# Optimization experiments

Hardware: AMD Instinct MI355X
Metric: run time of the kernel (lower is better)

The kernel has to match this reference:

```python
import jax, jax.numpy as jnp
from jax import lax
import numpy as np

H = 30          # LSTM_HID_SIZE
NOUT = 5        # ENC_NUM_OUT


def lstm_layer(x, W, b):
    """TF contrib LSTMCell over time. x: [B, T, D], W: [D+H, 4H] (i, j, f, o), forget_bias=1.0."""
    B = x.shape[0]
    c0 = jnp.zeros((B, H), x.dtype)
    h0 = jnp.zeros((B, H), x.dtype)

    def step(carry, xt):
        c, h = carry
        z = jnp.concatenate([xt, h], axis=-1) @ W + b
        i, j, f, o = jnp.split(z, 4, axis=-1)
        c = c * jax.nn.sigmoid(f + 1.0) + jax.nn.sigmoid(i) * jnp.tanh(j)
        h = jnp.tanh(c) * jax.nn.sigmoid(o)
        return (c, h), h

    _, hs = lax.scan(step, (c0, h0), jnp.swapaxes(x, 0, 1))  # hs: [T, B, H]
    return jnp.swapaxes(hs, 0, 1)


def setup_inputs() -> dict:
    key = jax.random.key(0)
    ks = jax.random.split(key, 13)
    B, T, D = 64, 2048, 256
    s = 0.1
    w = lambda k, shp: (jax.random.normal(k, shp, dtype=jnp.float32) * s)
    return {
        "seq": jax.random.normal(ks[0], (B, T, D), dtype=jnp.float32),
        # encoder stacked LSTM
        "enc_W1": w(ks[1], (D + H, 4 * H)), "enc_b1": jnp.zeros((4 * H,), jnp.float32),
        "enc_W2": w(ks[2], (H + H, 4 * H)), "enc_b2": jnp.zeros((4 * H,), jnp.float32),
        # encoder dense -> latent
        "enc_Wd": w(ks[3], (H, NOUT)), "enc_bd": jnp.zeros((NOUT,), jnp.float32),
        # decoder dense (dead code in original, kept for faithfulness)
        "dec_Wd": w(ks[4], (NOUT, NOUT)), "dec_bd": jnp.zeros((NOUT,), jnp.float32),
        # decoder stacked LSTM over zero inputs of width 1
        "dec_W1": w(ks[5], (1 + H, 4 * H)), "dec_b1": jnp.zeros((4 * H,), jnp.float32),
        "dec_W2": w(ks[6], (H + H, 4 * H)), "dec_b2": jnp.zeros((4 * H,), jnp.float32),
    }


def reference(seq, enc_W1, enc_b1, enc_W2, enc_b2, enc_Wd, enc_bd,
              dec_Wd, dec_bd, dec_W1, dec_b1, dec_W2, dec_b2):
    B, T, _ = seq.shape
    # ---- encoder: 2-layer LSTM, last timestep, tanh dense -> latent [B, 5]
    h1 = lstm_layer(seq, enc_W1, enc_b1)
    h2 = lstm_layer(h1, enc_W2, enc_b2)
    latent = jnp.tanh(h2[:, -1, :] @ enc_Wd + enc_bd)
    # ---- decoder dense on latent (unused downstream in the original graph)
    vec2 = jnp.tanh(latent @ dec_Wd + dec_bd)  # noqa: F841 (dead code, faithful to source)
    # ---- decoder: 2-layer LSTM over zeros [B, T, 1], zero initial state
    dec_in = jnp.zeros((B, T, 1), seq.dtype)
    d1 = lstm_layer(dec_in, dec_W1, dec_b1)
    d2 = lstm_layer(d1, dec_W2, dec_b2)
    dec_out = d2[:, :, -1]  # output[:, :, -1] -> [B, T]
    return dec_out, latent
```

## Files before the change

### kernel.cpp

```cpp
#include <hip/hip_runtime.h>


#define BB 64
#define TT 2048
#define DD 256
#define HH 30
#define GG 120
#define PRE_ELEMS (64u * 2048u * 120u)

__device__ __forceinline__ float fast_exp(float x) {
  return __builtin_amdgcn_exp2f(x * 1.442695040888963f);
}
__device__ __forceinline__ float fast_rcp(float x) {
  return __builtin_amdgcn_rcpf(x);
}
__device__ __forceinline__ float sigm(float x) {
  return fast_rcp(1.0f + fast_exp(-x));
}
__device__ __forceinline__ float tanh_f(float x) {
  return 1.0f - 2.0f * fast_rcp(1.0f + fast_exp(2.0f * x));
}

__global__ __launch_bounds__(256) void gemm_pre(const float* __restrict__ A,
                                                const float* __restrict__ W,
                                                const float* __restrict__ bias,
                                                float* __restrict__ out) {
  __shared__ __align__(16) float sA[32 * 132];
  __shared__ __align__(16) float sW[32 * 120];
  const int tid = threadIdx.x;
  const int row0 = blockIdx.x * 128;
  const int tx = tid % 30;
  const int ty = tid / 30;
  const bool comp = tid < 240;
  float4 acc[16];
#pragma unroll
  for (int i = 0; i < 16; ++i) acc[i] = make_float4(0.f, 0.f, 0.f, 0.f);
  const float4* A4 = (const float4*)A;
  const float4* W4 = (const float4*)W;
  const int rload = tid >> 3;
  const int kq = tid & 7;
  for (int k0 = 0; k0 < 256; k0 += 32) {
    __syncthreads();
#pragma unroll
    for (int it = 0; it < 4; ++it) {
      int idx = tid + it * 256;
      if (idx < 960) ((float4*)sW)[idx] = W4[k0 * 30 + idx];
    }
#pragma unroll
    for (int m = 0; m < 4; ++m) {
      int rr = rload + m * 32;
      float4 v = A4[(size_t)(row0 + rr) * 64 + (k0 >> 2) + kq];
      int kk = kq * 4;
      sA[(kk + 0) * 132 + rr] = v.x;
      sA[(kk + 1) * 132 + rr] = v.y;
      sA[(kk + 2) * 132 + rr] = v.z;
      sA[(kk + 3) * 132 + rr] = v.w;
    }
    __syncthreads();
    if (comp) {
#pragma unroll 4
      for (int k = 0; k < 32; ++k) {
        const float4 w = ((const float4*)sW)[k * 30 + tx];
        const float4* a4 = (const float4*)&sA[k * 132 + ty * 16];
        float4 a0 = a4[0], a1 = a4[1], a2 = a4[2], a3 = a4[3];
        float av[16] = {a0.x, a0.y, a0.z, a0.w, a1.x, a1.y, a1.z, a1.w,
                        a2.x, a2.y, a2.z, a2.w, a3.x, a3.y, a3.z, a3.w};
#pragma unroll
        for (int i = 0; i < 16; ++i) {
          acc[i].x = fmaf(av[i], w.x, acc[i].x);
          acc[i].y = fmaf(av[i], w.y, acc[i].y);
          acc[i].z = fmaf(av[i], w.z, acc[i].z);
          acc[i].w = fmaf(av[i], w.w, acc[i].w);
        }
      }
    }
  }
  if (comp) {
    const float4 bv = ((const float4*)bias)[tx];
#pragma unroll
    for (int i = 0; i < 16; ++i) {
      int row = row0 + ty * 16 + i;
      float4 r;
      r.x = acc[i].x + bv.x;
      r.y = acc[i].y + bv.y;
      r.z = acc[i].z + bv.z;
      r.w = acc[i].w + bv.w;
      ((float4*)out)[(size_t)row * 30 + tx] = r;
    }
  }
}

__global__ __launch_bounds__(128, 1) void scan_kernel(
    const float* __restrict__ pre, const float* __restrict__ enc_W1,
    const float* __restrict__ enc_W2, const float* __restrict__ enc_b2,
    const float* __restrict__ enc_Wd, const float* __restrict__ enc_bd,
    const float* __restrict__ dec_W1, const float* __restrict__ dec_b1,
    const float* __restrict__ dec_W2, const float* __restrict__ dec_b2,
    float* __restrict__ out, float* __restrict__ dec_seq) {
  __shared__ __align__(16) float h1buf[2][32];
  __shared__ __align__(16) float h2buf[32];
  const int tid = threadIdx.x;
  const int wave = tid >> 6;
  const int lane = tid & 63;
  const int blk = blockIdx.x;
  const bool isdec = (blk == BB);
  const bool act = lane < 60;
  if (tid < 32) {
    h1buf[0][tid] = 0.f;
    h1buf[1][tid] = 0.f;
    h2buf[tid] = 0.f;
  }
  float wA[60], wB[60];
  float biasA = 0.f, biasB = 0.f;
  float c = 0.f;
  const float* pr = pre + (size_t)blk * TT * GG;
  if (wave == 0) {
    const float* Wsrc = isdec ? (dec_W1 + GG) : (enc_W1 + 256 * GG);
    if (act) {
#pragma unroll
      for (int k = 0; k < 30; ++k) {
        wA[k] = Wsrc[k * GG + lane];
        wB[k] = Wsrc[k * GG + lane + 60];
      }
      if (isdec) {
        biasA = dec_b1[lane];
        biasB = dec_b1[lane + 60];
      }
    }
  } else {
    const float* Wsrc = isdec ? dec_W2 : enc_W2;
    const float* bsrc = isdec ? dec_b2 : enc_b2;
    if (act) {
#pragma unroll
      for (int k = 0; k < 60; ++k) {
        wA[k] = Wsrc[k * GG + lane];
        wB[k] = Wsrc[k * GG + lane + 60];
      }
      biasA = bsrc[lane];
      biasB = bsrc[lane + 60];
    }
  }
  float pA0 = biasA, pB0 = biasB, pA1 = biasA, pB1 = biasB;
  if (wave == 0 && !isdec && act) {
    pA0 = pr[lane];
    pB0 = pr[lane + 60];
    pA1 = pr[GG + lane];
    pB1 = pr[GG + lane + 60];
  }

  auto l1step = [&](int s, float& pa, float& pb) {
    const int rp = (s + 1) & 1, wp = s & 1;
    const float4* hp = (const float4*)&h1buf[rp][0];
    float4 q0 = hp[0], q1 = hp[1], q2 = hp[2], q3 = hp[3], q4 = hp[4], q5 = hp[5],
           q6 = hp[6], q7 = hp[7];
    float hv[32] = {q0.x, q0.y, q0.z, q0.w, q1.x, q1.y, q1.z, q1.w,
                    q2.x, q2.y, q2.z, q2.w, q3.x, q3.y, q3.z, q3.w,
                    q4.x, q4.y, q4.z, q4.w, q5.x, q5.y, q5.z, q5.w,
                    q6.x, q6.y, q6.z, q6.w, q7.x, q7.y, q7.z, q7.w};
    float aA = pa, aB = pb;
    if (!isdec && act) {
      int s2 = s + 2;
      if (s2 < TT) {
        pa = pr[s2 * GG + lane];
        pb = pr[s2 * GG + lane + 60];
      }
    }
#pragma unroll
    for (int k = 0; k < 30; ++k) {
      aA = fmaf(hv[k], wA[k], aA);
      aB = fmaf(hv[k], wB[k], aB);
    }
    float p1, p2;
    if (lane < 30) {
      p1 = sigm(aA);
      p2 = sigm(aB + 1.0f);
    } else {
      p1 = tanh_f(aA);
      p2 = sigm(aB);
    }
    float jv = __shfl(p1, lane + 30, 64);
    float ov = __shfl(p2, lane + 30, 64);
    if (lane < 30) {
      c = c * p2 + p1 * jv;
      float hnew = tanh_f(c) * ov;
      h1buf[wp][lane] = hnew;
    }
  };

  auto l2step = [&](int t) {
    const int rp = t & 1;
    const float4* hp1 = (const float4*)&h1buf[rp][0];
    const float4* hp2 = (const float4*)&h2buf[0];
    float4 q0 = hp1[0], q1 = hp1[1], q2 = hp1[2], q3 = hp1[3], q4 = hp1[4],
           q5 = hp1[5], q6 = hp1[6], q7 = hp1[7];
    float4 r0 = hp2[0], r1 = hp2[1], r2 = hp2[2], r3 = hp2[3], r4 = hp2[4],
           r5 = hp2[5], r6 = hp2[6], r7 = hp2[7];
    float h1v[32] = {q0.x, q0.y, q0.z, q0.w, q1.x, q1.y, q1.z, q1.w,
                     q2.x, q2.y, q2.z, q2.w, q3.x, q3.y, q3.z, q3.w,
                     q4.x, q4.y, q4.z, q4.w, q5.x, q5.y, q5.z, q5.w,
                     q6.x, q6.y, q6.z, q6.w, q7.x, q7.y, q7.z, q7.w};
    float h2v[32] = {r0.x, r0.y, r0.z, r0.w, r1.x, r1.y, r1.z, r1.w,
                     r2.x, r2.y, r2.z, r2.w, r3.x, r3.y, r3.z, r3.w,
                     r4.x, r4.y, r4.z, r4.w, r5.x, r5.y, r5.z, r5.w,
                     r6.x, r6.y, r6.z, r6.w, r7.x, r7.y, r7.z, r7.w};
    float aA = biasA, aB = biasB;
#pragma unroll
    for (int k = 0; k < 30; ++k) {
      aA = fmaf(h1v[k], wA[k], aA);
      aB = fmaf(h1v[k], wB[k], aB);
    }
#pragma unroll
    for (int k = 0; k < 30; ++k) {
      aA = fmaf(h2v[k], wA[30 + k], aA);
      aB = fmaf(h2v[k], wB[30 + k], aB);
    }
    float p1, p2;
    if (lane < 30) {
      p1 = sigm(aA);
      p2 = sigm(aB + 1.0f);
    } else {
      p1 = tanh_f(aA);
      p2 = sigm(aB);
    }
    float jv = __shfl(p1, lane + 30, 64);
    float ov = __shfl(p2, lane + 30, 64);
    if (lane < 30) {
      c = c * p2 + p1 * jv;
      float hnew = tanh_f(c) * ov;
      h2buf[lane] = hnew;
      if (isdec && lane == HH - 1) dec_seq[t] = hnew;
    }
  };

  for (int ss = 0; ss < TT; ss += 2) {
    __syncthreads();
    if (wave == 0) {
      l1step(ss, pA0, pB0);
    } else if (ss > 0) {
      l2step(ss - 1);
    }
    __syncthreads();
    if (wave == 0) {
      l1step(ss + 1, pA1, pB1);
    } else {
      l2step(ss);
    }
  }
  __syncthreads();
  if (wave == 1) {
    l2step(TT - 1);
    if (!isdec && lane < 5) {
      float a = enc_bd[lane];
#pragma unroll
      for (int k = 0; k < 30; ++k) a = fmaf(h2buf[k], enc_Wd[k * 5 + lane], a);
      out[BB * TT + blk * 5 + lane] = tanh_f(a);
    }
  }
}

__global__ __launch_bounds__(256) void bcast_kernel(const float* __restrict__ dec_seq,
                                                    float* __restrict__ out) {
  int i4 = blockIdx.x * 256 + threadIdx.x;
  ((float4*)out)[i4] = ((const float4*)dec_seq)[i4 & (TT / 4 - 1)];
}

extern "C" void kernel_launch(void* const* d_in, const int* in_sizes, int n_in,
                              void* d_out, int out_size, void* d_ws, size_t ws_size,
                              hipStream_t stream) {
  const float* seq = (const float*)d_in[0];
  const float* enc_W1 = (const float*)d_in[1];
  const float* enc_b1 = (const float*)d_in[2];
  const float* enc_W2 = (const float*)d_in[3];
  const float* enc_b2 = (const float*)d_in[4];
  const float* enc_Wd = (const float*)d_in[5];
  const float* enc_bd = (const float*)d_in[6];
  const float* dec_W1 = (const float*)d_in[9];
  const float* dec_b1 = (const float*)d_in[10];
  const float* dec_W2 = (const float*)d_in[11];
  const float* dec_b2 = (const float*)d_in[12];
  float* out = (float*)d_out;
  float* pre = (float*)d_ws;
  float* dec_seq = pre + PRE_ELEMS;

  gemm_pre<<<dim3(1024), dim3(256), 0, stream>>>(seq, enc_W1, enc_b1, pre);
  scan_kernel<<<dim3(65), dim3(128), 0, stream>>>(pre, enc_W1, enc_W2, enc_b2,
                                                  enc_Wd, enc_bd, dec_W1, dec_b1,
                                                  dec_W2, dec_b2, out, dec_seq);
  bcast_kernel<<<dim3(128), dim3(256), 0, stream>>>(dec_seq, out);
}
```

Measured before the change: 1.181 ms.

## Fuse both LSTM layers into one wave using readlane broadcasts instead of LDS

The scan kernel drops from two waves (one per layer, synchronised through shared-memory h buffers and __syncthreads) to a single 64-lane wave that computes both layers each step. Hidden state is broadcast with readlane into registers instead of LDS round-trips. Gate activations use lane-dependent constants so one branch-free formula covers sigmoid and tanh, and lanes are remapped to 32+32 halves so the exchange is a shfl_xor. The serial chain per step gets longer (layer-2 work is no longer overlapped with layer 1), and register pressure rises from holding all four weight sets, in exchange for removing the block barriers and LDS latency.

```diff
diff --git a/kernel.cpp b/kernel.cpp
--- a/kernel.cpp
+++ b/kernel.cpp
@@ -8,17 +8,13 @@
 #define GG 120
 #define PRE_ELEMS (64u * 2048u * 120u)
 
-__device__ __forceinline__ float fast_exp(float x) {
-  return __builtin_amdgcn_exp2f(x * 1.442695040888963f);
-}
-__device__ __forceinline__ float fast_rcp(float x) {
-  return __builtin_amdgcn_rcpf(x);
-}
-__device__ __forceinline__ float sigm(float x) {
-  return fast_rcp(1.0f + fast_exp(-x));
-}
+__device__ __forceinline__ float fast_exp2(float x) { return __builtin_amdgcn_exp2f(x); }
+__device__ __forceinline__ float fast_rcp(float x) { return __builtin_amdgcn_rcpf(x); }
 __device__ __forceinline__ float tanh_f(float x) {
-  return 1.0f - 2.0f * fast_rcp(1.0f + fast_exp(2.0f * x));
+  return 1.0f - 2.0f * fast_rcp(1.0f + fast_exp2(2.0f * 1.442695040888963f * x));
+}
+__device__ __forceinline__ float bcastf(float v, int l) {
+  return __builtin_bit_cast(float, __builtin_amdgcn_readlane(__builtin_bit_cast(int, v), l));
 }
 
 __global__ __launch_bounds__(256) void gemm_pre(const float* __restrict__ A,
@@ -90,170 +86,166 @@
   }
 }
 
-__global__ __launch_bounds__(128, 1) void scan_kernel(
+__global__ __launch_bounds__(64, 1) void scan_kernel(
     const float* __restrict__ pre, const float* __restrict__ enc_W1,
     const float* __restrict__ enc_W2, const float* __restrict__ enc_b2,
     const float* __restrict__ enc_Wd, const float* __restrict__ enc_bd,
     const float* __restrict__ dec_W1, const float* __restrict__ dec_b1,
     const float* __restrict__ dec_W2, const float* __restrict__ dec_b2,
     float* __restrict__ out, float* __restrict__ dec_seq) {
-  __shared__ __align__(16) float h1buf[2][32];
-  __shared__ __align__(16) float h2buf[32];
-  const int tid = threadIdx.x;
-  const int wave = tid >> 6;
-  const int lane = tid & 63;
+  const int lane = threadIdx.x;
   const int blk = blockIdx.x;
   const bool isdec = (blk == BB);
-  const bool act = lane < 60;
-  if (tid < 32) {
-    h1buf[0][tid] = 0.f;
-    h1buf[1][tid] = 0.f;
-    h2buf[tid] = 0.f;
-  }
-  float wA[60], wB[60];
-  float biasA = 0.f, biasB = 0.f;
-  float c = 0.f;
+  const int r = lane & 31;
+  const bool jo = lane >= 32;
+  const int cA = (r < 30) ? (jo ? 30 + r : r) : 0;
+  const int cB = cA + 60;
+
+  const float LOG2E = 1.442695040888963f;
+  const float m1 = jo ? 2.0f * LOG2E : -LOG2E;
+  const float A1 = jo ? -2.0f : 1.0f;
+  const float B1 = jo ? 1.0f : 0.0f;
+  const float fb = jo ? 0.0f : 1.0f;
+
+  float w1A[30], w1B[30], w2A[60], w2B[60];
+  {
+    const float* W1h = isdec ? (dec_W1 + GG) : (enc_W1 + 256 * GG);
+#pragma unroll
+    for (int k = 0; k < 30; ++k) {
+      w1A[k] = W1h[k * GG + cA];
+      w1B[k] = W1h[k * GG + cB];
+    }
+    const float* W2 = isdec ? dec_W2 : enc_W2;
+#pragma unroll
+    for (int k = 0; k < 60; ++k) {
+      w2A[k] = W2[k * GG + cA];
+      w2B[k] = W2[k * GG + cB];
+    }
+  }
+  const float* b2 = isdec ? dec_b2 : enc_b2;
+  const float b2A = b2[cA], b2B = b2[cB];
+
   const float* pr = pre + (size_t)blk * TT * GG;
-  if (wave == 0) {
-    const float* Wsrc = isdec ? (dec_W1 + GG) : (enc_W1 + 256 * GG);
-    if (act) {
-#pragma unroll
-      for (int k = 0; k < 30; ++k) {
-        wA[k] = Wsrc[k * GG + lane];
-        wB[k] = Wsrc[k * GG + lane + 60];
-      }
-      if (isdec) {
-        biasA = dec_b1[lane];
-        biasB = dec_b1[lane + 60];
-      }
-    }
+  float pcurA, pcurB, pnxtA, pnxtB;
+  if (isdec) {
+    pcurA = dec_b1[cA];
+    pcurB = dec_b1[cB];
+    pnxtA = pcurA;
+    pnxtB = pcurB;
   } else {
-    const float* Wsrc = isdec ? dec_W2 : enc_W2;
-    const float* bsrc = isdec ? dec_b2 : enc_b2;
-    if (act) {
-#pragma unroll
-      for (int k = 0; k < 60; ++k) {
-        wA[k] = Wsrc[k * GG + lane];
-        wB[k] = Wsrc[k * GG + lane + 60];
-      }
-      biasA = bsrc[lane];
-      biasB = bsrc[lane + 60];
-    }
-  }
-  float pA0 = biasA, pB0 = biasB, pA1 = biasA, pB1 = biasB;
-  if (wave == 0 && !isdec && act) {
-    pA0 = pr[lane];
-    pB0 = pr[lane + 60];
-    pA1 = pr[GG + lane];
-    pB1 = pr[GG + lane + 60];
-  }
-
-  auto l1step = [&](int s, float& pa, float& pb) {
-    const int rp = (s + 1) & 1, wp = s & 1;
-    const float4* hp = (const float4*)&h1buf[rp][0];
-    float4 q0 = hp[0], q1 = hp[1], q2 = hp[2], q3 = hp[3], q4 = hp[4], q5 = hp[5],
-           q6 = hp[6], q7 = hp[7];
-    float hv[32] = {q0.x, q0.y, q0.z, q0.w, q1.x, q1.y, q1.z, q1.w,
-                    q2.x, q2.y, q2.z, q2.w, q3.x, q3.y, q3.z, q3.w,
-                    q4.x, q4.y, q4.z, q4.w, q5.x, q5.y, q5.z, q5.w,
-                    q6.x, q6.y, q6.z, q6.w, q7.x, q7.y, q7.z, q7.w};
-    float aA = pa, aB = pb;
-    if (!isdec && act) {
+    pcurA = pr[cA];
+    pcurB = pr[cB];
+    pnxtA = pr[GG + cA];
+    pnxtB = pr[GG + cB];
+  }
+
+  float sv1[30], sv2[30];
+#pragma unroll
+  for (int k = 0; k < 30; ++k) sv2[k] = 0.f;
+
+  float c1 = 0.f, c2 = 0.f, h1r, h2r;
+
+  {
+    float t1 = fast_rcp(1.0f + fast_exp2(pcurA * m1));
+    float p1 = fmaf(t1, A1, B1);
+    float p2 = fast_rcp(1.0f + fast_exp2((pcurB + fb) * -LOG2E));
+    float jv = __shfl_xor(p1, 32, 64);
+    float ov = __shfl_xor(p2, 32, 64);
+    c1 = p1 * jv;
+    h1r = tanh_f(c1) * ov;
+#pragma unroll
+    for (int k = 0; k < 30; ++k) sv1[k] = bcastf(h1r, k);
+    pcurA = pnxtA;
+    pcurB = pnxtB;
+    if (!isdec) {
+      pnxtA = pr[2 * GG + cA];
+      pnxtB = pr[2 * GG + cB];
+    }
+  }
+
+  for (int s = 1; s < TT; ++s) {
+    float aA = pcurA, aB = pcurB;
+    float bA = b2A, bB = b2B;
+    float pldA = pnxtA, pldB = pnxtB;
+    if (!isdec) {
       int s2 = s + 2;
       if (s2 < TT) {
-        pa = pr[s2 * GG + lane];
-        pb = pr[s2 * GG + lane + 60];
+        pldA = pr[(size_t)s2 * GG + cA];
+        pldB = pr[(size_t)s2 * GG + cB];
       }
     }
 #pragma unroll
     for (int k = 0; k < 30; ++k) {
-      aA = fmaf(hv[k], wA[k], aA);
-      aB = fmaf(hv[k], wB[k], aB);
-    }
-    float p1, p2;
-    if (lane < 30) {
-      p1 = sigm(aA);
-      p2 = sigm(aB + 1.0f);
+      float hk = sv1[k];
+      aA = fmaf(hk, w1A[k], aA);
+      aB = fmaf(hk, w1B[k], aB);
+      bA = fmaf(hk, w2A[k], bA);
+      bB = fmaf(hk, w2B[k], bB);
+    }
+#pragma unroll
+    for (int k = 0; k < 30; ++k) {
+      float hk = sv2[k];
+      bA = fmaf(hk, w2A[30 + k], bA);
+      bB = fmaf(hk, w2B[30 + k], bB);
+    }
+    {
+      float t1 = fast_rcp(1.0f + fast_exp2(aA * m1));
+      float p1 = fmaf(t1, A1, B1);
+      float p2 = fast_rcp(1.0f + fast_exp2((aB + fb) * -LOG2E));
+      float jv = __shfl_xor(p1, 32, 64);
+      float ov = __shfl_xor(p2, 32, 64);
+      c1 = fmaf(c1, p2, p1 * jv);
+      h1r = tanh_f(c1) * ov;
+    }
+#pragma unroll
+    for (int k = 0; k < 30; ++k) sv1[k] = bcastf(h1r, k);
+    {
+      float u1 = fast_rcp(1.0f + fast_exp2(bA * m1));
+      float q1 = fmaf(u1, A1, B1);
+      float q2 = fast_rcp(1.0f + fast_exp2((bB + fb) * -LOG2E));
+      float jw = __shfl_xor(q1, 32, 64);
+      float ow = __shfl_xor(q2, 32, 64);
+      c2 = fmaf(c2, q2, q1 * jw);
+      h2r = tanh_f(c2) * ow;
+    }
+    if (isdec && lane == HH - 1) dec_seq[s - 1] = h2r;
+#pragma unroll
+    for (int k = 0; k < 30; ++k) sv2[k] = bcastf(h2r, k);
+    pcurA = pnxtA;
+    pcurB = pnxtB;
+    pnxtA = pldA;
+    pnxtB = pldB;
+  }
+
+  {
+    float bA = b2A, bB = b2B;
+#pragma unroll
+    for (int k = 0; k < 30; ++k) {
+      float hk = sv1[k];
+      bA = fmaf(hk, w2A[k], bA);
+      bB = fmaf(hk, w2B[k], bB);
+    }
+#pragma unroll
+    for (int k = 0; k < 30; ++k) {
+      float hk = sv2[k];
+      bA = fmaf(hk, w2A[30 + k], bA);
+      bB = fmaf(hk, w2B[30 + k], bB);
+    }
+    float u1 = fast_rcp(1.0f + fast_exp2(bA * m1));
+    float q1 = fmaf(u1, A1, B1);
+    float q2 = fast_rcp(1.0f + fast_exp2((bB + fb) * -LOG2E));
+    float jw = __shfl_xor(q1, 32, 64);
+    float ow = __shfl_xor(q2, 32, 64);
+    c2 = fmaf(c2, q2, q1 * jw);
+    h2r = tanh_f(c2) * ow;
+    if (isdec) {
+      if (lane == HH - 1) dec_seq[TT - 1] = h2r;
     } else {
-      p1 = tanh_f(aA);
-      p2 = sigm(aB);
-    }
-    float jv = __shfl(p1, lane + 30, 64);
-    float ov = __shfl(p2, lane + 30, 64);
-    if (lane < 30) {
-      c = c * p2 + p1 * jv;
-      float hnew = tanh_f(c) * ov;
-      h1buf[wp][lane] = hnew;
-    }
-  };
-
-  auto l2step = [&](int t) {
-    const int rp = t & 1;
-    const float4* hp1 = (const float4*)&h1buf[rp][0];
-    const float4* hp2 = (const float4*)&h2buf[0];
-    float4 q0 = hp1[0], q1 = hp1[1], q2 = hp1[2], q3 = hp1[3], q4 = hp1[4],
-           q5 = hp1[5], q6 = hp1[6], q7 = hp1[7];
-    float4 r0 = hp2[0], r1 = hp2[1], r2 = hp2[2], r3 = hp2[3], r4 = hp2[4],
-           r5 = hp2[5], r6 = hp2[6], r7 = hp2[7];
-    float h1v[32] = {q0.x, q0.y, q0.z, q0.w, q1.x, q1.y, q1.z, q1.w,
-                     q2.x, q2.y, q2.z, q2.w, q3.x, q3.y, q3.z, q3.w,
-                     q4.x, q4.y, q4.z, q4.w, q5.x, q5.y, q5.z, q5.w,
-                     q6.x, q6.y, q6.z, q6.w, q7.x, q7.y, q7.z, q7.w};
-    float h2v[32] = {r0.x, r0.y, r0.z, r0.w, r1.x, r1.y, r1.z, r1.w,
-                     r2.x, r2.y, r2.z, r2.w, r3.x, r3.y, r3.z, r3.w,
-                     r4.x, r4.y, r4.z, r4.w, r5.x, r5.y, r5.z, r5.w,
-                     r6.x, r6.y, r6.z, r6.w, r7.x, r7.y, r7.z, r7.w};
-    float aA = biasA, aB = biasB;
-#pragma unroll
-    for (int k = 0; k < 30; ++k) {
-      aA = fmaf(h1v[k], wA[k], aA);
-      aB = fmaf(h1v[k], wB[k], aB);
-    }
-#pragma unroll
-    for (int k = 0; k < 30; ++k) {
-      aA = fmaf(h2v[k], wA[30 + k], aA);
-      aB = fmaf(h2v[k], wB[30 + k], aB);
-    }
-    float p1, p2;
-    if (lane < 30) {
-      p1 = sigm(aA);
-      p2 = sigm(aB + 1.0f);
-    } else {
-      p1 = tanh_f(aA);
-      p2 = sigm(aB);
-    }
-    float jv = __shfl(p1, lane + 30, 64);
-    float ov = __shfl(p2, lane + 30, 64);
-    if (lane < 30) {
-      c = c * p2 + p1 * jv;
-      float hnew = tanh_f(c) * ov;
-      h2buf[lane] = hnew;
-      if (isdec && lane == HH - 1) dec_seq[t] = hnew;
-    }
-  };
-
-  for (int ss = 0; ss < TT; ss += 2) {
-    __syncthreads();
-    if (wave == 0) {
-      l1step(ss, pA0, pB0);
-    } else if (ss > 0) {
-      l2step(ss - 1);
-    }
-    __syncthreads();
-    if (wave == 0) {
-      l1step(ss + 1, pA1, pB1);
-    } else {
-      l2step(ss);
-    }
-  }
-  __syncthreads();
-  if (wave == 1) {
-    l2step(TT - 1);
-    if (!isdec && lane < 5) {
-      float a = enc_bd[lane];
-#pragma unroll
-      for (int k = 0; k < 30; ++k) a = fmaf(h2buf[k], enc_Wd[k * 5 + lane], a);
-      out[BB * TT + blk * 5 + lane] = tanh_f(a);
+      float a = enc_bd[lane < 5 ? lane : 0];
+#pragma unroll
+      for (int k = 0; k < 30; ++k)
+        a = fmaf(bcastf(h2r, k), enc_Wd[k * 5 + (lane < 5 ? lane : 0)], a);
+      if (lane < 5) out[BB * TT + blk * 5 + lane] = tanh_f(a);
     }
   }
 }
@@ -283,8 +275,8 @@
   float* dec_seq = pre + PRE_ELEMS;
 
   gemm_pre<<<dim3(1024), dim3(256), 0, stream>>>(seq, enc_W1, enc_b1, pre);
-  scan_kernel<<<dim3(65), dim3(128), 0, stream>>>(pre, enc_W1, enc_W2, enc_b2,
-                                                  enc_Wd, enc_bd, dec_W1, dec_b1,
-                                                  dec_W2, dec_b2, out, dec_seq);
+  scan_kernel<<<dim3(65), dim3(64), 0, stream>>>(pre, enc_W1, enc_W2, enc_b2,
+                                                 enc_Wd, enc_bd, dec_W1, dec_b1,
+                                                 dec_W2, dec_b2, out, dec_seq);
   bcast_kernel<<<dim3(128), dim3(256), 0, stream>>>(dec_seq, out);
 }
```

Result: slower. 1.535 ms (+29.9%).
